# Kernel optimization log

Hardware: AMD Instinct MI355X
Metric: run time of the kernel (lower is better)

Reference implementation:

```python
import jax, jax.numpy as jnp
import numpy as np

DILATION = 1   # -> kernel k = 3 + 2*(d-1) = 3, pad = d
THETA = 1.0
EPS_LOG = 1e-5
EPS_STD = 1e-3
EXP_MAX = 15.0


def setup_inputs() -> dict:
    key = jax.random.key(0)
    x = jax.random.uniform(key, (8, 64, 128, 128), dtype=jnp.float32)
    return {"x": x}


def _extract_patches(x, d):
    # x: [B, C, H, W] -> patches [B, C, 9, H, W], zero-padded 3x3 dilated window
    B, C, H, W = x.shape
    xp = jnp.pad(x, ((0, 0), (0, 0), (d, d), (d, d)))
    slices = [xp[:, :, i * d:i * d + H, j * d:j * d + W]
              for i in range(3) for j in range(3)]
    return jnp.stack(slices, axis=2)


def reference(x):
    B, C, H, W = x.shape
    patches = _extract_patches(x, DILATION)  # [B, C, K=9, H, W]
    K = patches.shape[2]

    mean = patches.mean(axis=2, keepdims=True)
    centered = patches - mean
    # torch .std() is unbiased (ddof=1), then clamped to 1e-3
    var = (centered ** 2).sum(axis=2, keepdims=True) / (K - 1)
    std = jnp.maximum(jnp.sqrt(var), EPS_STD)
    normed = centered / std

    contrast = (normed ** 2).mean(axis=2)                       # [B, C, H, W]
    energy = (patches ** 2).mean(axis=2)
    cl = jnp.maximum(patches, 1e-6)
    entropy = -(cl * jnp.log(cl)).mean(axis=2)
    homogeneity = 1.0 / ((1.0 + jnp.abs(centered)).mean(axis=2) + 1e-6)

    # feature order matches dict iteration: contrast, energy, entropy, homogeneity
    feats = jnp.stack([contrast, energy, entropy, homogeneity], axis=2)  # [B, C, 4, H, W]

    # martingale transform: M = exp(clamp(theta*log(clamp(f)) - 0.5*theta^2, max=15))
    log_f = jnp.log(jnp.maximum(feats, EPS_LOG))
    M = jnp.exp(jnp.minimum(THETA * log_f - 0.5 * THETA ** 2, EXP_MAX))
    M = jnp.clip(M, 1e-4, 1e4)
    M = jnp.where(jnp.isfinite(M), M, jnp.ones_like(M))

    # per-channel features are contiguous: channel c -> out[:, 4c:4c+4]
    return M.reshape(B, C * 4, H, W)
```

## Files before the change

### kernel.cpp

```cpp
#include <hip/hip_runtime.h>


#define Wd 128
#define Hd 128
#define HWd 16384

typedef float v4f __attribute__((ext_vector_type(4)));

__device__ __forceinline__ float mart(float f) {
    float fc = fmaxf(f, 1e-5f);
    float M = fc * 0.60653065971263342f;
    return fminf(fmaxf(M, 1e-4f), 1e4f);
}

__global__ __launch_bounds__(256) void medseg_kernel(const float* __restrict__ x,
                                                     float* __restrict__ out) {
    int tid = blockIdx.x * 256 + threadIdx.x;
    int plane = tid >> 12;
    int rem = tid & 4095;
    int h = rem >> 5;
    int lane31 = rem & 31;
    int w0 = lane31 << 2;

    const float* xp = x + (size_t)plane * HWd;

    v4f v[3];
#pragma unroll
    for (int dr = 0; dr < 3; ++dr) {
        int hh = h + dr - 1;
        if (hh < 0 || hh >= Hd) {
            v[dr] = (v4f){0.f, 0.f, 0.f, 0.f};
        } else {
            v[dr] = *reinterpret_cast<const v4f*>(xp + hh * Wd + w0);
        }
    }

    float r[3][6];
#pragma unroll
    for (int dr = 0; dr < 3; ++dr) {
        float left  = __shfl_up(v[dr].w, 1);
        float right = __shfl_down(v[dr].x, 1);
        r[dr][0] = (lane31 == 0)  ? 0.f : left;
        r[dr][1] = v[dr].x; r[dr][2] = v[dr].y; r[dr][3] = v[dr].z; r[dr][4] = v[dr].w;
        r[dr][5] = (lane31 == 31) ? 0.f : right;
    }

    float colS[6], colE[6], colN[6];
#pragma unroll
    for (int j = 0; j < 6; ++j) {
        float s = 0.f, e = 0.f, en = 0.f;
#pragma unroll
        for (int dr = 0; dr < 3; ++dr) {
            float vv = r[dr][j];
            s += vv;
            e = fmaf(vv, vv, e);
            float cl = fmaxf(vv, 1e-6f);
            en = fmaf(cl, __logf(cl), en);
        }
        colS[j] = s; colE[j] = e; colN[j] = en;
    }

    float con[4], ene[4], ent[4], hom[4];
#pragma unroll
    for (int i = 0; i < 4; ++i) {
        float sum = colS[i] + colS[i + 1] + colS[i + 2];
        float m = sum * (1.f / 9.f);
        float energy = (colE[i] + colE[i + 1] + colE[i + 2]) * (1.f / 9.f);
        float entropy = -(colN[i] + colN[i + 1] + colN[i + 2]) * (1.f / 9.f);

        float s2 = 0.f, sa = 0.f;
#pragma unroll
        for (int dr = 0; dr < 3; ++dr) {
#pragma unroll
            for (int dj = 0; dj < 3; ++dj) {
                float c = r[dr][i + dj] - m;
                s2 = fmaf(c, c, s2);
                sa += fabsf(c);
            }
        }
        float var = s2 * 0.125f;
        float sd = fmaxf(sqrtf(var), 1e-3f);
        float contrast = s2 * (1.f / 9.f) / (sd * sd);
        float homog = 1.f / ((9.f + sa) * (1.f / 9.f) + 1e-6f);

        con[i] = mart(contrast);
        ene[i] = mart(energy);
        ent[i] = mart(entropy);
        hom[i] = mart(homog);
    }

    size_t base = (size_t)plane * 4 * HWd + h * Wd + w0;
    __builtin_nontemporal_store((v4f){con[0], con[1], con[2], con[3]},
                                reinterpret_cast<v4f*>(out + base));
    __builtin_nontemporal_store((v4f){ene[0], ene[1], ene[2], ene[3]},
                                reinterpret_cast<v4f*>(out + base + HWd));
    __builtin_nontemporal_store((v4f){ent[0], ent[1], ent[2], ent[3]},
                                reinterpret_cast<v4f*>(out + base + 2 * HWd));
    __builtin_nontemporal_store((v4f){hom[0], hom[1], hom[2], hom[3]},
                                reinterpret_cast<v4f*>(out + base + 3 * HWd));
}

extern "C" void kernel_launch(void* const* d_in, const int* in_sizes, int n_in,
                              void* d_out, int out_size, void* d_ws, size_t ws_size,
                              hipStream_t stream) {
    const float* x = (const float*)d_in[0];
    float* out = (float*)d_out;
    int n_planes = in_sizes[0] / HWd;
    int total_threads = n_planes * (HWd / 4);
    int blocks = total_threads / 256;
    medseg_kernel<<<blocks, 256, 0, stream>>>(x, out);
}
```

Before: 160.2 us.

## Process eight pixels per thread and compute variance from sum and energy

Each thread now loads two float4 vectors per row and computes eight outputs instead of four. This amortizes the column sums, log evaluations and halo shuffles over more pixels, and halves the thread count. The centered squared sum is now derived algebraically as E9 - mean*sum instead of a second 9-tap pass, which removes some arithmetic. In exchange it uses more registers and adds fp32 cancellation risk in the variance, clamped at zero.

```diff
diff --git a/kernel.cpp b/kernel.cpp
--- a/kernel.cpp
+++ b/kernel.cpp
@@ -16,38 +16,42 @@
 __global__ __launch_bounds__(256) void medseg_kernel(const float* __restrict__ x,
                                                      float* __restrict__ out) {
     int tid = blockIdx.x * 256 + threadIdx.x;
-    int plane = tid >> 12;
-    int rem = tid & 4095;
-    int h = rem >> 5;
-    int lane31 = rem & 31;
-    int w0 = lane31 << 2;
+    int plane = tid >> 11;
+    int rem = tid & 2047;
+    int h = rem >> 4;
+    int lane15 = rem & 15;
+    int w0 = lane15 << 3;
 
     const float* xp = x + (size_t)plane * HWd;
 
-    v4f v[3];
+    v4f a[3], b[3];
 #pragma unroll
     for (int dr = 0; dr < 3; ++dr) {
         int hh = h + dr - 1;
         if (hh < 0 || hh >= Hd) {
-            v[dr] = (v4f){0.f, 0.f, 0.f, 0.f};
+            a[dr] = (v4f){0.f, 0.f, 0.f, 0.f};
+            b[dr] = (v4f){0.f, 0.f, 0.f, 0.f};
         } else {
-            v[dr] = *reinterpret_cast<const v4f*>(xp + hh * Wd + w0);
+            const float* row = xp + hh * Wd + w0;
+            a[dr] = *reinterpret_cast<const v4f*>(row);
+            b[dr] = *reinterpret_cast<const v4f*>(row + 4);
         }
     }
 
-    float r[3][6];
+    float r[3][10];
 #pragma unroll
     for (int dr = 0; dr < 3; ++dr) {
-        float left  = __shfl_up(v[dr].w, 1);
-        float right = __shfl_down(v[dr].x, 1);
-        r[dr][0] = (lane31 == 0)  ? 0.f : left;
-        r[dr][1] = v[dr].x; r[dr][2] = v[dr].y; r[dr][3] = v[dr].z; r[dr][4] = v[dr].w;
-        r[dr][5] = (lane31 == 31) ? 0.f : right;
+        float left  = __shfl_up(b[dr].w, 1);
+        float right = __shfl_down(a[dr].x, 1);
+        r[dr][0] = (lane15 == 0)  ? 0.f : left;
+        r[dr][1] = a[dr].x; r[dr][2] = a[dr].y; r[dr][3] = a[dr].z; r[dr][4] = a[dr].w;
+        r[dr][5] = b[dr].x; r[dr][6] = b[dr].y; r[dr][7] = b[dr].z; r[dr][8] = b[dr].w;
+        r[dr][9] = (lane15 == 15) ? 0.f : right;
     }
 
-    float colS[6], colE[6], colN[6];
+    float colS[10], colE[10], colN[10];
 #pragma unroll
-    for (int j = 0; j < 6; ++j) {
+    for (int j = 0; j < 10; ++j) {
         float s = 0.f, e = 0.f, en = 0.f;
 #pragma unroll
         for (int dr = 0; dr < 3; ++dr) {
@@ -60,44 +64,49 @@
         colS[j] = s; colE[j] = e; colN[j] = en;
     }
 
-    float con[4], ene[4], ent[4], hom[4];
+    size_t base = (size_t)plane * 4 * HWd + h * Wd + w0;
+
 #pragma unroll
-    for (int i = 0; i < 4; ++i) {
-        float sum = colS[i] + colS[i + 1] + colS[i + 2];
-        float m = sum * (1.f / 9.f);
-        float energy = (colE[i] + colE[i + 1] + colE[i + 2]) * (1.f / 9.f);
-        float entropy = -(colN[i] + colN[i + 1] + colN[i + 2]) * (1.f / 9.f);
+    for (int half = 0; half < 2; ++half) {
+        float con[4], ene[4], ent[4], hom[4];
+#pragma unroll
+        for (int k = 0; k < 4; ++k) {
+            int i = half * 4 + k;
+            float sum = colS[i] + colS[i + 1] + colS[i + 2];
+            float m = sum * (1.f / 9.f);
+            float E9 = colE[i] + colE[i + 1] + colE[i + 2];
+            float energy = E9 * (1.f / 9.f);
+            float entropy = -(colN[i] + colN[i + 1] + colN[i + 2]) * (1.f / 9.f);
 
-        float s2 = 0.f, sa = 0.f;
+            float s2 = fmaxf(fmaf(-m, sum, E9), 0.f);
+
+            float sa = 0.f;
 #pragma unroll
-        for (int dr = 0; dr < 3; ++dr) {
+            for (int dr = 0; dr < 3; ++dr) {
 #pragma unroll
-            for (int dj = 0; dj < 3; ++dj) {
-                float c = r[dr][i + dj] - m;
-                s2 = fmaf(c, c, s2);
-                sa += fabsf(c);
+                for (int dj = 0; dj < 3; ++dj)
+                    sa += fabsf(r[dr][i + dj] - m);
             }
+            float var = s2 * 0.125f;
+            float sd = fmaxf(sqrtf(var), 1e-3f);
+            float contrast = s2 * (1.f / 9.f) / (sd * sd);
+            float homog = 1.f / ((9.f + sa) * (1.f / 9.f) + 1e-6f);
+
+            con[k] = mart(contrast);
+            ene[k] = mart(energy);
+            ent[k] = mart(entropy);
+            hom[k] = mart(homog);
         }
-        float var = s2 * 0.125f;
-        float sd = fmaxf(sqrtf(var), 1e-3f);
-        float contrast = s2 * (1.f / 9.f) / (sd * sd);
-        float homog = 1.f / ((9.f + sa) * (1.f / 9.f) + 1e-6f);
-
-        con[i] = mart(contrast);
-        ene[i] = mart(energy);
-        ent[i] = mart(entropy);
-        hom[i] = mart(homog);
+        size_t o = base + half * 4;
+        __builtin_nontemporal_store((v4f){con[0], con[1], con[2], con[3]},
+                                    reinterpret_cast<v4f*>(out + o));
+        __builtin_nontemporal_store((v4f){ene[0], ene[1], ene[2], ene[3]},
+                                    reinterpret_cast<v4f*>(out + o + HWd));
+        __builtin_nontemporal_store((v4f){ent[0], ent[1], ent[2], ent[3]},
+                                    reinterpret_cast<v4f*>(out + o + 2 * HWd));
+        __builtin_nontemporal_store((v4f){hom[0], hom[1], hom[2], hom[3]},
+                                    reinterpret_cast<v4f*>(out + o + 3 * HWd));
     }
-
-    size_t base = (size_t)plane * 4 * HWd + h * Wd + w0;
-    __builtin_nontemporal_store((v4f){con[0], con[1], con[2], con[3]},
-                                reinterpret_cast<v4f*>(out + base));
-    __builtin_nontemporal_store((v4f){ene[0], ene[1], ene[2], ene[3]},
-                                reinterpret_cast<v4f*>(out + base + HWd));
-    __builtin_nontemporal_store((v4f){ent[0], ent[1], ent[2], ent[3]},
-                                reinterpret_cast<v4f*>(out + base + 2 * HWd));
-    __builtin_nontemporal_store((v4f){hom[0], hom[1], hom[2], hom[3]},
-                                reinterpret_cast<v4f*>(out + base + 3 * HWd));
 }
 
 extern "C" void kernel_launch(void* const* d_in, const int* in_sizes, int n_in,
@@ -106,7 +115,7 @@
     const float* x = (const float*)d_in[0];
     float* out = (float*)d_out;
     int n_planes = in_sizes[0] / HWd;
-    int total_threads = n_planes * (HWd / 4);
+    int total_threads = n_planes * (HWd / 8);
     int blocks = total_threads / 256;
     medseg_kernel<<<blocks, 256, 0, stream>>>(x, out);
 }
```

Result: slower. 224.0 us (+39.8%).

## Compute two output rows per thread and derive variance from sums

Applied to the files above, without the earlier changes.

Each thread now handles a 2x4 output tile. It loads four input rows instead of three and shares the middle two rows' column sums, squares and log terms between both outputs, which halves the thread count and cuts redundant loads and log evaluations. The centred squared sum is now computed algebraically as E9 - m*sum, clamped at zero, instead of being accumulated directly. That formula can lose precision through cancellation, and the larger per-thread tile raises register pressure.

```diff
diff --git a/kernel.cpp b/kernel.cpp
--- a/kernel.cpp
+++ b/kernel.cpp
@@ -16,17 +16,18 @@
 __global__ __launch_bounds__(256) void medseg_kernel(const float* __restrict__ x,
                                                      float* __restrict__ out) {
     int tid = blockIdx.x * 256 + threadIdx.x;
-    int plane = tid >> 12;
-    int rem = tid & 4095;
-    int h = rem >> 5;
+    int plane = tid >> 11;
+    int rem = tid & 2047;
+    int h2 = rem >> 5;
     int lane31 = rem & 31;
     int w0 = lane31 << 2;
+    int h = h2 << 1;
 
     const float* xp = x + (size_t)plane * HWd;
 
-    v4f v[3];
+    v4f v[4];
 #pragma unroll
-    for (int dr = 0; dr < 3; ++dr) {
+    for (int dr = 0; dr < 4; ++dr) {
         int hh = h + dr - 1;
         if (hh < 0 || hh >= Hd) {
             v[dr] = (v4f){0.f, 0.f, 0.f, 0.f};
@@ -35,9 +36,9 @@
         }
     }
 
-    float r[3][6];
+    float r[4][6];
 #pragma unroll
-    for (int dr = 0; dr < 3; ++dr) {
+    for (int dr = 0; dr < 4; ++dr) {
         float left  = __shfl_up(v[dr].w, 1);
         float right = __shfl_down(v[dr].x, 1);
         r[dr][0] = (lane31 == 0)  ? 0.f : left;
@@ -45,59 +46,67 @@
         r[dr][5] = (lane31 == 31) ? 0.f : right;
     }
 
-    float colS[6], colE[6], colN[6];
+    float colS[2][6], colE[2][6], colN[2][6];
 #pragma unroll
     for (int j = 0; j < 6; ++j) {
-        float s = 0.f, e = 0.f, en = 0.f;
+        float e[4], n[4];
 #pragma unroll
-        for (int dr = 0; dr < 3; ++dr) {
+        for (int dr = 0; dr < 4; ++dr) {
             float vv = r[dr][j];
-            s += vv;
-            e = fmaf(vv, vv, e);
+            e[dr] = vv * vv;
             float cl = fmaxf(vv, 1e-6f);
-            en = fmaf(cl, __logf(cl), en);
+            n[dr] = cl * __logf(cl);
         }
-        colS[j] = s; colE[j] = e; colN[j] = en;
-    }
-
-    float con[4], ene[4], ent[4], hom[4];
-#pragma unroll
-    for (int i = 0; i < 4; ++i) {
-        float sum = colS[i] + colS[i + 1] + colS[i + 2];
-        float m = sum * (1.f / 9.f);
-        float energy = (colE[i] + colE[i + 1] + colE[i + 2]) * (1.f / 9.f);
-        float entropy = -(colN[i] + colN[i + 1] + colN[i + 2]) * (1.f / 9.f);
-
-        float s2 = 0.f, sa = 0.f;
-#pragma unroll
-        for (int dr = 0; dr < 3; ++dr) {
-#pragma unroll
-            for (int dj = 0; dj < 3; ++dj) {
-                float c = r[dr][i + dj] - m;
-                s2 = fmaf(c, c, s2);
-                sa += fabsf(c);
-            }
-        }
-        float var = s2 * 0.125f;
-        float sd = fmaxf(sqrtf(var), 1e-3f);
-        float contrast = s2 * (1.f / 9.f) / (sd * sd);
-        float homog = 1.f / ((9.f + sa) * (1.f / 9.f) + 1e-6f);
-
-        con[i] = mart(contrast);
-        ene[i] = mart(energy);
-        ent[i] = mart(entropy);
-        hom[i] = mart(homog);
+        float s12 = r[1][j] + r[2][j];
+        float e12 = e[1] + e[2];
+        float n12 = n[1] + n[2];
+        colS[0][j] = r[0][j] + s12;  colS[1][j] = s12 + r[3][j];
+        colE[0][j] = e[0] + e12;     colE[1][j] = e12 + e[3];
+        colN[0][j] = n[0] + n12;     colN[1][j] = n12 + n[3];
     }
 
     size_t base = (size_t)plane * 4 * HWd + h * Wd + w0;
-    __builtin_nontemporal_store((v4f){con[0], con[1], con[2], con[3]},
-                                reinterpret_cast<v4f*>(out + base));
-    __builtin_nontemporal_store((v4f){ene[0], ene[1], ene[2], ene[3]},
-                                reinterpret_cast<v4f*>(out + base + HWd));
-    __builtin_nontemporal_store((v4f){ent[0], ent[1], ent[2], ent[3]},
-                                reinterpret_cast<v4f*>(out + base + 2 * HWd));
-    __builtin_nontemporal_store((v4f){hom[0], hom[1], hom[2], hom[3]},
-                                reinterpret_cast<v4f*>(out + base + 3 * HWd));
+
+#pragma unroll
+    for (int rs = 0; rs < 2; ++rs) {
+        float con[4], ene[4], ent[4], hom[4];
+#pragma unroll
+        for (int i = 0; i < 4; ++i) {
+            float sum = colS[rs][i] + colS[rs][i + 1] + colS[rs][i + 2];
+            float m = sum * (1.f / 9.f);
+            float E9 = colE[rs][i] + colE[rs][i + 1] + colE[rs][i + 2];
+            float energy = E9 * (1.f / 9.f);
+            float entropy = -(colN[rs][i] + colN[rs][i + 1] + colN[rs][i + 2]) * (1.f / 9.f);
+
+            float s2 = fmaxf(fmaf(-m, sum, E9), 0.f);
+
+            float sa = 0.f;
+#pragma unroll
+            for (int dr = 0; dr < 3; ++dr) {
+#pragma unroll
+                for (int dj = 0; dj < 3; ++dj)
+                    sa += fabsf(r[rs + dr][i + dj] - m);
+            }
+            float var = s2 * 0.125f;
+            float sd = fmaxf(sqrtf(var), 1e-3f);
+            float contrast = s2 * (1.f / 9.f) / (sd * sd);
+            float homog = 1.f / ((9.f + sa) * (1.f / 9.f) + 1e-6f);
+
+            con[i] = mart(contrast);
+            ene[i] = mart(energy);
+            ent[i] = mart(entropy);
+            hom[i] = mart(homog);
+        }
+        size_t o = base + rs * Wd;
+        __builtin_nontemporal_store((v4f){con[0], con[1], con[2], con[3]},
+                                    reinterpret_cast<v4f*>(out + o));
+        __builtin_nontemporal_store((v4f){ene[0], ene[1], ene[2], ene[3]},
+                                    reinterpret_cast<v4f*>(out + o + HWd));
+        __builtin_nontemporal_store((v4f){ent[0], ent[1], ent[2], ent[3]},
+                                    reinterpret_cast<v4f*>(out + o + 2 * HWd));
+        __builtin_nontemporal_store((v4f){hom[0], hom[1], hom[2], hom[3]},
+                                    reinterpret_cast<v4f*>(out + o + 3 * HWd));
+    }
 }
 
 extern "C" void kernel_launch(void* const* d_in, const int* in_sizes, int n_in,
@@ -106,7 +115,7 @@
     const float* x = (const float*)d_in[0];
     float* out = (float*)d_out;
     int n_planes = in_sizes[0] / HWd;
-    int total_threads = n_planes * (HWd / 4);
+    int total_threads = n_planes * (HWd / 8);
     int blocks = total_threads / 256;
     medseg_kernel<<<blocks, 256, 0, stream>>>(x, out);
 }
```

New measurement: 157.4 us. No clear change (-1.7%).
